# Kernel tuning notes

Hardware: AMD Instinct MI355X
Metric: run time of the kernel (lower is better)

The kernel has to match this reference:

```python
import jax, jax.numpy as jnp
import numpy as np

B, S, H, D, M = 4, 512, 768, 24, 96
OUT_HID = 2 * max(128, H // 2)  # 768

def setup_inputs() -> dict:
    key = jax.random.key(0)
    ks = jax.random.split(key, 10)
    g = lambda k, shp, s=0.02: (jax.random.normal(k, shp, jnp.float32) * s)
    return {
        'H_j': jax.random.normal(ks[0], (B, S, H), jnp.float32),
        'H_i': jax.random.normal(ks[1], (B, S, H), jnp.float32),
        'attn_mask': jnp.ones((B, S), jnp.float32),
        'p_j_w': g(ks[2], (D, H)),
        'p_i_w': g(ks[3], (D, H)),
        's_w1': g(ks[4], (M, 4 * D)),
        's_b1': jnp.zeros((M,), jnp.float32),
        's_w2': g(ks[5], (1, M)),
        's_b2': jnp.zeros((1,), jnp.float32),
        'v_w1': g(ks[6], (OUT_HID, 3 * H)),
        'v_b1': jnp.zeros((OUT_HID,), jnp.float32),
        'v_w2': g(ks[7], (H, OUT_HID)),
        'v_b2': jnp.zeros((H,), jnp.float32),
        'alpha': jnp.asarray(0.05, jnp.float32),
    }

def reference(H_j, H_i, attn_mask, p_j_w, p_i_w, s_w1, s_b1, s_w2, s_b2,
              v_w1, v_b1, v_w2, v_b2, alpha):
    # Projections: [B,S,D]
    Zj = H_j @ p_j_w.T
    Zi = H_i @ p_i_w.T
    # score_mlp layer1 on concat([Zj_pair, Zi_pair, hadam, |diff|]) ==
    # sum of the 4 block-matmuls (block-split of W1 over the concat axis).
    Wa, Wb, Wc, Wd = jnp.split(s_w1, 4, axis=1)        # each [M, D]
    Zj_p = Zj[:, :, None, :]                            # [B,S,1,D]
    Zi_p = Zi[:, None, :, :]                            # [B,1,S,D]
    hid = (jnp.einsum('bsd,md->bsm', Zj, Wa)[:, :, None, :]
           + jnp.einsum('btd,md->btm', Zi, Wb)[:, None, :, :]
           + jnp.einsum('bstd,md->bstm', Zj_p * Zi_p, Wc)
           + jnp.einsum('bstd,md->bstm', jnp.abs(Zj_p - Zi_p), Wd)
           + s_b1)                                      # [B,S,S,M]
    logits = jnp.einsum('bstm,om->bst', jax.nn.relu(hid), s_w2)[..., :] + s_b2[0]  # [B,S,S]
    neg = jnp.finfo(logits.dtype).min
    logits = logits + (1.0 - attn_mask)[:, None, :] * neg  # mask over keys
    probs = jax.nn.softmax(logits, axis=-1)
    ctx = jnp.einsum('bst,bth->bsh', probs, H_i)           # [B,S,H]
    msg_in = jnp.concatenate([ctx, H_j, ctx * H_j], axis=-1)  # concat_hadam: [B,S,3H]
    msg = jax.nn.relu(msg_in @ v_w1.T + v_b1) @ v_w2.T + v_b2
    return alpha * msg  # dropout is identity in eval mode
```

## Files before the change

### kernel.cpp

```cpp
#include <hip/hip_runtime.h>
#include <hip/hip_bf16.h>
#include <math.h>

#define BB 4
#define SS 512
#define HH 768
#define DD 24
#define MM 96
#define OH 768
#define K3H 2304

typedef unsigned short u16;
typedef unsigned int u32;
typedef short bf16x8 __attribute__((ext_vector_type(8)));
typedef float f32x4 __attribute__((ext_vector_type(4)));
typedef u16 u16x4 __attribute__((ext_vector_type(4)));

#define MB_MSGIN  0
#define MB_H1     (MB_MSGIN + BB*SS*K3H)
#define MB_W1     (MB_H1    + BB*SS*OH)
#define MB_W2     (MB_W1    + OH*K3H)
#define MB_PROBS  (MB_W2    + OH*HH)
#define MB_HIT    (MB_PROBS + BB*SS*SS)
#define MB_ZJP    (MB_HIT   + BB*HH*SS)
#define MB_ZIP    (MB_ZJP   + BB*SS*32)
#define MB_WM     (MB_ZIP   + BB*SS*32)
#define MB_WAB    (MB_WM    + MM*96)
#define MB_AB     (MB_WAB   + MM*32)

__device__ inline u16 f2bf(float x) {
    union { float f; u32 u; } v; v.f = x;
    u32 r = v.u + 0x7fffu + ((v.u >> 16) & 1u);
    return (u16)(r >> 16);
}
__device__ inline u32 pk2bf(float lo, float hi) {
    return ((__float_as_uint(lo) + 0x8000u) >> 16) |
           ((__float_as_uint(hi) + 0x8000u) & 0xffff0000u);
}
__device__ inline void unpack8(bf16x8 v, float* f) {
    const u32* d = (const u32*)&v;
    #pragma unroll
    for (int i = 0; i < 4; ++i) {
        f[2*i]   = __uint_as_float(d[i] << 16);
        f[2*i+1] = __uint_as_float(d[i] & 0xffff0000u);
    }
}
__device__ inline void gl_lds16(const u16* g, u16* l) {
    __builtin_amdgcn_global_load_lds(
        (const __attribute__((address_space(1))) void*)g,
        (__attribute__((address_space(3))) void*)l, 16, 0, 0);
}
__device__ inline bf16x8 frag64(const u16* X, int r, int g) {
    return *(const bf16x8*)&X[(r*8 + (g ^ (r & 7)))*8];
}

__global__ __launch_bounds__(256) void k_wm(
    const float* __restrict__ sw1, u16* __restrict__ Wm, u16* __restrict__ Wab)
{
    for (int i = threadIdx.x; i < MM*96; i += 256) {
        int m = i / 96, k = i % 96;
        float v = 0.f;
        if (k < 24)                 v = sw1[m*96 + 48 + k];
        else if (k >= 32 && k < 56) v = sw1[m*96 + 72 + (k - 32)];
        else if (k >= 64 && k < 88) v = sw1[m*96 + 24 + (k - 64)];
        Wm[i] = f2bf(v);
    }
    for (int i = threadIdx.x; i < MM*32; i += 256) {
        int m = i >> 5, k = i & 31;
        Wab[i] = (k < 24) ? f2bf(sw1[m*96 + k]) : (u16)0;
    }
}

#define PZ_END   64
#define PC1_END  928
#define PC2_END  1216
#define PHJ_END  1984
#define PHT_END  2368

__global__ __launch_bounds__(256) void k_prep(
    const float* __restrict__ Hj, const float* __restrict__ Hi,
    const float* __restrict__ pjw, const float* __restrict__ piw,
    const float* __restrict__ sb1,
    const float* __restrict__ vw1, const float* __restrict__ vw2,
    const u16* __restrict__ Wab,
    u16* __restrict__ w1b, u16* __restrict__ w2b,
    u16* __restrict__ Zjp, u16* __restrict__ Zip, u16* __restrict__ Ab,
    u16* __restrict__ msginb, u16* __restrict__ HiTb)
{
    __shared__ __align__(16) u16 smem[5120];
    int bx = blockIdx.x;
    int tid = threadIdx.x;

    if (bx < PZ_END) {
        int idx = bx;
        int isJ = (idx < 32);
        int n0 = (idx & 31) * 64;
        const float* H = isJ ? Hj : Hi;
        const float* P = isJ ? pjw : piw;
        u16* Zout = isJ ? Zjp : Zip;
        u16* As = smem;
        u16* Bs = smem + 2048;
        u16* zb = smem + 3072;
        int wave = tid >> 6, lane = tid & 63;
        int q = lane >> 4, l16 = lane & 15;

        { int i = tid; Bs[(24 + (i >> 5))*32 + (i & 31)] = 0; }

        int arow = tid >> 2, aseg = tid & 3;
        const float* ah = H + (size_t)(n0 + arow)*HH + aseg*8;
        const float* bh = P + (size_t)arow*HH + aseg*8;
        int adst = arow*32 + ((aseg ^ (arow & 3))*8);

        float4 xa = *(const float4*)(ah);
        float4 ya = *(const float4*)(ah + 4);
        float4 xb = {}, yb = {};
        if (tid < 96) { xb = *(const float4*)(bh); yb = *(const float4*)(bh + 4); }

        f32x4 acc0 = {}, acc1 = {};
        int ga = q ^ (l16 & 3);
        for (int k0 = 0; k0 < HH; k0 += 32) {
            { u32* w = (u32*)&As[adst];
              w[0] = pk2bf(xa.x, xa.y); w[1] = pk2bf(xa.z, xa.w);
              w[2] = pk2bf(ya.x, ya.y); w[3] = pk2bf(ya.z, ya.w); }
            if (tid < 96) {
              u32* w = (u32*)&Bs[adst];
              w[0] = pk2bf(xb.x, xb.y); w[1] = pk2bf(xb.z, xb.w);
              w[2] = pk2bf(yb.x, yb.y); w[3] = pk2bf(yb.z, yb.w); }
            float4 nxa = {}, nya = {}, nxb = {}, nyb = {};
            if (k0 + 32 < HH) {
                nxa = *(const float4*)(ah + k0 + 32);
                nya = *(const float4*)(ah + k0 + 36);
                if (tid < 96) { nxb = *(const float4*)(bh + k0 + 32);
                                nyb = *(const float4*)(bh + k0 + 36); }
            }
            __syncthreads();
            bf16x8 af = *(const bf16x8*)&As[(wave*16 + l16)*32 + ga*8];
            bf16x8 b0 = *(const bf16x8*)&Bs[l16*32 + ga*8];
            bf16x8 b1 = *(const bf16x8*)&Bs[(16 + l16)*32 + ga*8];
            acc0 = __builtin_amdgcn_mfma_f32_16x16x32_bf16(af, b0, acc0, 0,0,0);
            acc1 = __builtin_amdgcn_mfma_f32_16x16x32_bf16(af, b1, acc1, 0,0,0);
            __syncthreads();
            xa = nxa; ya = nya; xb = nxb; yb = nyb;
        }
        #pragma unroll
        for (int r = 0; r < 4; ++r) {
            zb[(wave*16 + q*4 + r)*32 + l16]      = f2bf(acc0[r]);
            zb[(wave*16 + q*4 + r)*32 + 16 + l16] = f2bf(acc1[r]);
        }
        __syncthreads();
        { uint4 v = *(const uint4*)&zb[tid*8];
          *(uint4*)&Zout[(size_t)n0*32 + tid*8] = v; }
        if (isJ) {
            bf16x8 af = *(const bf16x8*)&zb[(wave*16 + l16)*32 + q*8];
            #pragma unroll
            for (int nt = 0; nt < 6; ++nt) {
                bf16x8 bw = *(const bf16x8*)&Wab[(nt*16 + l16)*32 + q*8];
                f32x4 a = {};
                a = __builtin_amdgcn_mfma_f32_16x16x32_bf16(af, bw, a, 0,0,0);
                float bv = sb1[nt*16 + l16];
                #pragma unroll
                for (int r = 0; r < 4; ++r) {
                    int bs = n0 + wave*16 + q*4 + r;
                    Ab[(size_t)bs*MM + nt*16 + l16] = f2bf(a[r] + bv);
                }
            }
        }
    } else if (bx < PC2_END) {
        int idx; const float* src; u16* dst;
        if (bx < PC1_END) { idx = bx - PZ_END;  src = vw1; dst = w1b; }
        else              { idx = bx - PC1_END; src = vw2; dst = w2b; }
        int i = (idx*256 + tid) * 8;
        float4 a = *(const float4*)&src[i];
        float4 c = *(const float4*)&src[i+4];
        u16x4 lo = { f2bf(a.x), f2bf(a.y), f2bf(a.z), f2bf(a.w) };
        u16x4 hi = { f2bf(c.x), f2bf(c.y), f2bf(c.z), f2bf(c.w) };
        *(u16x4*)&dst[i]   = lo;
        *(u16x4*)&dst[i+4] = hi;
    } else if (bx < PHJ_END) {
        int idx = bx - PC2_END;
        int e = (idx*256 + tid) * 8;
        int n = e / HH, k = e - n*HH;
        float4 a = *(const float4*)&Hj[e];
        float4 c = *(const float4*)&Hj[e+4];
        u16* dst = msginb + (size_t)n*K3H + HH + k;
        u16x4 lo = { f2bf(a.x), f2bf(a.y), f2bf(a.z), f2bf(a.w) };
        u16x4 hi = { f2bf(c.x), f2bf(c.y), f2bf(c.z), f2bf(c.w) };
        *(u16x4*)&dst[0] = lo;
        *(u16x4*)&dst[4] = hi;
    } else {
        int idx = bx - PHJ_END;
        int t0 = (idx & 7) * 64;
        int h0 = ((idx >> 3) % 12) * 64;
        int b  = idx / 96;
        u16* tile = smem;
        int r = tid >> 2, cs = tid & 3;
        const float* src = Hi + ((size_t)(b*SS) + t0 + r)*HH + h0 + cs*16;
        u16* dst = &tile[r*74 + cs*16];
        #pragma unroll
        for (int i = 0; i < 4; ++i) {
            float4 v = *(const float4*)(src + i*4);
            *(u32*)&dst[i*4]     = pk2bf(v.x, v.y);
            *(u32*)&dst[i*4 + 2] = pk2bf(v.z, v.w);
        }
        __syncthreads();
        int hr = tid >> 2;
        u16 outv[16];
        #pragma unroll
        for (int i = 0; i < 16; ++i) outv[i] = tile[(cs*16 + i)*74 + hr];
        u16* o = HiTb + ((size_t)b*HH + h0 + hr)*SS + t0 + cs*16;
        *(uint4*)o       = *(const uint4*)&outv[0];
        *(uint4*)(o + 8) = *(const uint4*)&outv[8];
    }
}

__global__ __launch_bounds__(256) void k_pair_mfma(
    const u16* __restrict__ Zjp, const u16* __restrict__ Zip,
    const u16* __restrict__ Ab, const u16* __restrict__ Wm,
    const float* __restrict__ sw2, const float* __restrict__ mask,
    u16* __restrict__ probsb)
{
    int blk = blockIdx.x; int b = blk >> 8; int s0 = (blk & 255) * 2;
    int tid = threadIdx.x, wave = tid >> 6, lane = tid & 63;
    int q = lane >> 4, l16 = lane & 15;
    int si = wave & 1, half = wave >> 1;
    int s = s0 + si, bs = b*SS + s;
    __shared__ __align__(16) u16 ZiS[SS*32];
    __shared__ float logits[2][SS];

    {
        const u16* zb = Zip + (size_t)b*SS*32;
        #pragma unroll
        for (int p = 0; p < 8; ++p) {
            int idx = p*256 + tid;
            int t = idx >> 2, c = idx & 3;
            int g = c ^ ((t + (t >> 2)) & 3);
            gl_lds16(zb + t*32 + g*8, ZiS + idx*8);
        }
    }

    bf16x8 zjf = *(const bf16x8*)&Zjp[(size_t)bs*32 + q*8];
    float zj[8]; unpack8(zjf, zj);
    bf16x8 afc[6], afd[6];
    #pragma unroll
    for (int mt = 0; mt < 6; ++mt) {
        const u16* wrow = &Wm[(mt*16 + l16)*96];
        bf16x8 wcf = *(const bf16x8*)&wrow[q*8];
        afd[mt]    = *(const bf16x8*)&wrow[32 + q*8];
        bf16x8 wbf = *(const bf16x8*)&wrow[64 + q*8];
        float fc[8], fb[8];
        unpack8(wcf, fc); unpack8(wbf, fb);
        u32 aval = (u32)Ab[(size_t)bs*MM + mt*16 + l16];
        union { u32 d[4]; bf16x8 v; } pk;
        #pragma unroll
        for (int i = 0; i < 4; ++i)
            pk.d[i] = pk2bf(fmaf(fc[2*i], zj[2*i], fb[2*i]),
                            fmaf(fc[2*i+1], zj[2*i+1], fb[2*i+1]));
        pk.d[0] = (q == 3) ? aval : pk.d[0];
        afc[mt] = pk.v;
    }
    float w2v[6][4];
    #pragma unroll
    for (int mt = 0; mt < 6; ++mt)
        #pragma unroll
        for (int r = 0; r < 4; ++r) w2v[mt][r] = sw2[mt*16 + q*4 + r];

    __syncthreads();

    for (int k = 0; k < 16; ++k) {
        int t0 = (half*16 + k) * 16;
        int trow = t0 + l16;
        int sw = q ^ ((trow + (trow >> 2)) & 3);
        bf16x8 zif = *(const bf16x8*)&ZiS[trow*32 + sw*8];
        float zi[8]; unpack8(zif, zi);
        union { u32 d[4]; bf16x8 v; } b1, b2;
        #pragma unroll
        for (int i = 0; i < 4; ++i)
            b1.d[i] = pk2bf(fabsf(zj[2*i] - zi[2*i]), fabsf(zj[2*i+1] - zi[2*i+1]));
        b2.v = zif;
        b2.d[0] = (q == 3) ? 0x3F80u : b2.d[0];
        f32x4 acc[6];
        #pragma unroll
        for (int mt = 0; mt < 6; ++mt) {
            f32x4 a = {};
            a = __builtin_amdgcn_mfma_f32_16x16x32_bf16(afc[mt], b2.v, a, 0,0,0);
            a = __builtin_amdgcn_mfma_f32_16x16x32_bf16(afd[mt], b1.v, a, 0,0,0);
            acc[mt] = a;
        }
        float p = 0.f;
        #pragma unroll
        for (int mt = 0; mt < 6; ++mt)
            #pragma unroll
            for (int r = 0; r < 4; ++r)
                p = fmaf(fmaxf(acc[mt][r], 0.f), w2v[mt][r], p);
        p += __shfl_xor(p, 16);
        p += __shfl_xor(p, 32);
        if (lane < 16) logits[si][t0 + lane] = p;
    }
    __syncthreads();

    if (wave < 2) {
        const float NEGF = -3.4028234663852886e38f;
        int bss = b*SS + s0 + wave;
        float l[8], e[8];
        float mx = -INFINITY;
        #pragma unroll
        for (int i = 0; i < 8; ++i) {
            int idx = lane + i*64;
            l[i] = logits[wave][idx] + (1.f - mask[b*SS + idx]) * NEGF;
            mx = fmaxf(mx, l[i]);
        }
        #pragma unroll
        for (int off = 32; off > 0; off >>= 1) mx = fmaxf(mx, __shfl_xor(mx, off));
        float sum = 0.f;
        #pragma unroll
        for (int i = 0; i < 8; ++i) { e[i] = __expf(l[i] - mx); sum += e[i]; }
        #pragma unroll
        for (int off = 32; off > 0; off >>= 1) sum += __shfl_xor(sum, off);
        float inv = 1.f / sum;
        #pragma unroll
        for (int i = 0; i < 8; ++i)
            probsb[(size_t)bss*SS + lane + i*64] = f2bf(e[i] * inv);
    }
}

__global__ __launch_bounds__(256) void k_ctx_mfma(
    const u16* __restrict__ probsb, const u16* __restrict__ HiTb,
    u16* __restrict__ msginb)
{
    int b = blockIdx.z;
    int h0 = blockIdx.x * 64;
    int s0 = blockIdx.y * 64;
    int tid = threadIdx.x;
    __shared__ __align__(16) u16 smem[8192];
    u16* As = smem;
    u16* Bs = smem + 4096;
    int wave = tid >> 6, lane = tid & 63;
    int wr = (wave >> 1) * 32, wc = (wave & 1) * 32;
    int q = lane >> 4, l16 = lane & 15;
    f32x4 acc[2][2] = {};
    const u16* ag = probsb + ((size_t)(b*SS) + s0)*SS;
    const u16* bg = HiTb + ((size_t)b*HH + h0)*SS;
    for (int k0 = 0; k0 < SS; k0 += 64) {
        #pragma unroll
        for (int p = 0; p < 2; ++p) {
            int sl = p*256 + tid; int rr = sl >> 3, gi = sl & 7, g = gi ^ (rr & 7);
            gl_lds16(ag + (size_t)rr*SS + k0 + g*8, As + sl*8);
            gl_lds16(bg + (size_t)rr*SS + k0 + g*8, Bs + sl*8);
        }
        __syncthreads();
        #pragma unroll
        for (int ks = 0; ks < 2; ++ks) {
            int g = ks*4 + q;
            bf16x8 a0 = frag64(As, wr + l16, g);
            bf16x8 a1 = frag64(As, wr + 16 + l16, g);
            bf16x8 b0 = frag64(Bs, wc + l16, g);
            bf16x8 b1 = frag64(Bs, wc + 16 + l16, g);
            acc[0][0] = __builtin_amdgcn_mfma_f32_16x16x32_bf16(a0, b0, acc[0][0], 0,0,0);
            acc[0][1] = __builtin_amdgcn_mfma_f32_16x16x32_bf16(a0, b1, acc[0][1], 0,0,0);
            acc[1][0] = __builtin_amdgcn_mfma_f32_16x16x32_bf16(a1, b0, acc[1][0], 0,0,0);
            acc[1][1] = __builtin_amdgcn_mfma_f32_16x16x32_bf16(a1, b1, acc[1][1], 0,0,0);
        }
        __syncthreads();
    }
    u16* zb = smem;
    #pragma unroll
    for (int rt = 0; rt < 2; ++rt)
        #pragma unroll
        for (int ct = 0; ct < 2; ++ct) {
            int hl = wc + ct*16 + l16;
            #pragma unroll
            for (int r = 0; r < 4; ++r)
                zb[(wr + rt*16 + q*4 + r)*72 + hl] = f2bf(acc[rt][ct][r]);
        }
    __syncthreads();
    {
        int s_l = tid >> 2, seg = tid & 3;
        u16 cv[16], hv[16], pv[16];
        *(uint4*)&cv[0] = *(const uint4*)&zb[s_l*72 + seg*16];
        *(uint4*)&cv[8] = *(const uint4*)&zb[s_l*72 + seg*16 + 8];
        u16* row = msginb + (size_t)(b*SS + s0 + s_l)*K3H;
        int hc = h0 + seg*16;
        *(uint4*)&hv[0] = *(const uint4*)&row[HH + hc];
        *(uint4*)&hv[8] = *(const uint4*)&row[HH + hc + 8];
        #pragma unroll
        for (int i = 0; i < 8; ++i) {
            float c0 = __uint_as_float((u32)cv[2*i] << 16);
            float c1 = __uint_as_float((u32)cv[2*i+1] << 16);
            float g0 = __uint_as_float((u32)hv[2*i] << 16);
            float g1 = __uint_as_float((u32)hv[2*i+1] << 16);
            u32 pr = pk2bf(c0*g0, c1*g1);
            pv[2*i] = (u16)pr; pv[2*i+1] = (u16)(pr >> 16);
        }
        *(uint4*)&row[hc]     = *(const uint4*)&cv[0];
        *(uint4*)&row[hc + 8] = *(const uint4*)&cv[8];
        *(uint4*)&row[2*HH + hc]     = *(const uint4*)&pv[0];
        *(uint4*)&row[2*HH + hc + 8] = *(const uint4*)&pv[8];
    }
}

__global__ __launch_bounds__(256) void k_mfma_gemm1(
    const u16* __restrict__ Abf, const u16* __restrict__ Bbf,
    const float* __restrict__ bias, u16* __restrict__ Cbf)
{
    int o0 = blockIdx.x * 64;
    int n0 = blockIdx.y * 64;
    int tid = threadIdx.x;
    __shared__ __align__(16) u16 As[64*64];
    __shared__ __align__(16) u16 Bs[64*64];
    int wave = tid >> 6, lane = tid & 63;
    int wr = (wave >> 1) * 32, wc = (wave & 1) * 32;
    int q = lane >> 4, l16 = lane & 15;
    f32x4 acc[2][2] = {};
    const u16* ag = Abf + (size_t)n0*K3H;
    const u16* bg = Bbf + (size_t)o0*K3H;
    for (int k0 = 0; k0 < K3H; k0 += 64) {
        #pragma unroll
        for (int p = 0; p < 2; ++p) {
            int sl = p*256 + tid; int rr = sl >> 3, gi = sl & 7, g = gi ^ (rr & 7);
            gl_lds16(ag + (size_t)rr*K3H + k0 + g*8, As + sl*8);
            gl_lds16(bg + (size_t)rr*K3H + k0 + g*8, Bs + sl*8);
        }
        __syncthreads();
        #pragma unroll
        for (int ks = 0; ks < 2; ++ks) {
            int g = ks*4 + q;
            bf16x8 a0 = frag64(As, wr + l16, g);
            bf16x8 a1 = frag64(As, wr + 16 + l16, g);
            bf16x8 b0 = frag64(Bs, wc + l16, g);
            bf16x8 b1 = frag64(Bs, wc + 16 + l16, g);
            acc[0][0] = __builtin_amdgcn_mfma_f32_16x16x32_bf16(a0, b0, acc[0][0], 0,0,0);
            acc[0][1] = __builtin_amdgcn_mfma_f32_16x16x32_bf16(a0, b1, acc[0][1], 0,0,0);
            acc[1][0] = __builtin_amdgcn_mfma_f32_16x16x32_bf16(a1, b0, acc[1][0], 0,0,0);
            acc[1][1] = __builtin_amdgcn_mfma_f32_16x16x32_bf16(a1, b1, acc[1][1], 0,0,0);
        }
        __syncthreads();
    }
    #pragma unroll
    for (int rt = 0; rt < 2; ++rt) {
        #pragma unroll
        for (int ct = 0; ct < 2; ++ct) {
            int o = o0 + wc + ct*16 + l16;
            float bv = bias[o];
            #pragma unroll
            for (int r = 0; r < 4; ++r) {
                int m = n0 + wr + rt*16 + q*4 + r;
                Cbf[(size_t)m*OH + o] = f2bf(fmaxf(acc[rt][ct][r] + bv, 0.f));
            }
        }
    }
}

__global__ __launch_bounds__(256) void k_mfma_gemm2(
    const u16* __restrict__ Abf, const u16* __restrict__ Bbf,
    const float* __restrict__ bias, const float* __restrict__ alpha,
    float* __restrict__ out)
{
    int o0 = blockIdx.x * 64;
    int n0 = blockIdx.y * 64;
    int tid = threadIdx.x;
    __shared__ __align__(16) u16 As[64*64];
    __shared__ __align__(16) u16 Bs[64*64];
    int wave = tid >> 6, lane = tid & 63;
    int wr = (wave >> 1) * 32, wc = (wave & 1) * 32;
    int q = lane >> 4, l16 = lane & 15;
    f32x4 acc[2][2] = {};
    const u16* ag = Abf + (size_t)n0*OH;
    const u16* bg = Bbf + (size_t)o0*OH;
    for (int k0 = 0; k0 < OH; k0 += 64) {
        #pragma unroll
        for (int p = 0; p < 2; ++p) {
            int sl = p*256 + tid; int rr = sl >> 3, gi = sl & 7, g = gi ^ (rr & 7);
            gl_lds16(ag + (size_t)rr*OH + k0 + g*8, As + sl*8);
            gl_lds16(bg + (size_t)rr*OH + k0 + g*8, Bs + sl*8);
        }
        __syncthreads();
        #pragma unroll
        for (int ks = 0; ks < 2; ++ks) {
            int g = ks*4 + q;
            bf16x8 a0 = frag64(As, wr + l16, g);
            bf16x8 a1 = frag64(As, wr + 16 + l16, g);
            bf16x8 b0 = frag64(Bs, wc + l16, g);
            bf16x8 b1 = frag64(Bs, wc + 16 + l16, g);
            acc[0][0] = __builtin_amdgcn_mfma_f32_16x16x32_bf16(a0, b0, acc[0][0], 0,0,0);
            acc[0][1] = __builtin_amdgcn_mfma_f32_16x16x32_bf16(a0, b1, acc[0][1], 0,0,0);
            acc[1][0] = __builtin_amdgcn_mfma_f32_16x16x32_bf16(a1, b0, acc[1][0], 0,0,0);
            acc[1][1] = __builtin_amdgcn_mfma_f32_16x16x32_bf16(a1, b1, acc[1][1], 0,0,0);
        }
        __syncthreads();
    }
    float al = alpha[0];
    #pragma unroll
    for (int rt = 0; rt < 2; ++rt) {
        #pragma unroll
        for (int ct = 0; ct < 2; ++ct) {
            int o = o0 + wc + ct*16 + l16;
            float bv = bias[o];
            #pragma unroll
            for (int r = 0; r < 4; ++r) {
                int m = n0 + wr + rt*16 + q*4 + r;
                out[(size_t)m*HH + o] = al * (acc[rt][ct][r] + bv);
            }
        }
    }
}

extern "C" void kernel_launch(void* const* d_in, const int* in_sizes, int n_in,
                              void* d_out, int out_size, void* d_ws, size_t ws_size,
                              hipStream_t stream) {
    const float* Hj    = (const float*)d_in[0];
    const float* Hi    = (const float*)d_in[1];
    const float* amask = (const float*)d_in[2];
    const float* pjw   = (const float*)d_in[3];
    const float* piw   = (const float*)d_in[4];
    const float* sw1   = (const float*)d_in[5];
    const float* sb1   = (const float*)d_in[6];
    const float* sw2   = (const float*)d_in[7];
    const float* sb2   = (const float*)d_in[8];
    const float* vw1   = (const float*)d_in[9];
    const float* vb1   = (const float*)d_in[10];
    const float* vw2   = (const float*)d_in[11];
    const float* vb2   = (const float*)d_in[12];
    const float* alpha = (const float*)d_in[13];
    float* out = (float*)d_out;
    (void)sb2;

    u16* bfbase = (u16*)d_ws;
    u16* msginb = bfbase + MB_MSGIN;
    u16* h1b    = bfbase + MB_H1;
    u16* w1b    = bfbase + MB_W1;
    u16* w2b    = bfbase + MB_W2;
    u16* probsb = bfbase + MB_PROBS;
    u16* hitb   = bfbase + MB_HIT;
    u16* zjp    = bfbase + MB_ZJP;
    u16* zip    = bfbase + MB_ZIP;
    u16* wm     = bfbase + MB_WM;
    u16* wab    = bfbase + MB_WAB;
    u16* ab     = bfbase + MB_AB;

    k_wm<<<1, 256, 0, stream>>>(sw1, wm, wab);
    k_prep<<<PHT_END, 256, 0, stream>>>(Hj, Hi, pjw, piw, sb1, vw1, vw2, wab,
                                        w1b, w2b, zjp, zip, ab, msginb, hitb);
    k_pair_mfma<<<BB*SS/2, 256, 0, stream>>>(zjp, zip, ab, wm, sw2, amask, probsb);
    k_ctx_mfma<<<dim3(HH/64, SS/64, BB), 256, 0, stream>>>(probsb, hitb, msginb);
    k_mfma_gemm1<<<dim3(OH/64, BB*SS/64), 256, 0, stream>>>(msginb, w1b, vb1, h1b);
    k_mfma_gemm2<<<dim3(HH/64, BB*SS/64), 256, 0, stream>>>(h1b, w2b, vb2, alpha, out);
}
```

Before: 191.0 us.

## Load GEMM B fragments directly from global and fuse Hj bf16 conversion into ctx

The three MFMA GEMM kernels no longer stage the B operand in LDS. Each wave now reads its bf16x8 B fragments straight from global memory, relying on L2/cache reuse across blocks and cutting LDS traffic and footprint. Separately, the Hj-to-bf16 copy into msg_in is removed from the prep kernel and done in the ctx epilogue, which reads fp32 Hj directly and writes all three msg_in segments. This drops a launch slice and a round trip through msg_in, but the B loads become uncoalesced, strided per-lane global reads inside the inner loop.

Result: slower. 229.1 us (+19.9%).

```diff
diff --git a/kernel.cpp b/kernel.cpp
--- a/kernel.cpp
+++ b/kernel.cpp
@@ -74,8 +74,7 @@
 #define PZ_END   64
 #define PC1_END  928
 #define PC2_END  1216
-#define PHJ_END  1984
-#define PHT_END  2368
+#define PHT_END  1600
 
 __global__ __launch_bounds__(256) void k_prep(
     const float* __restrict__ Hj, const float* __restrict__ Hi,
@@ -85,7 +84,7 @@
     const u16* __restrict__ Wab,
     u16* __restrict__ w1b, u16* __restrict__ w2b,
     u16* __restrict__ Zjp, u16* __restrict__ Zip, u16* __restrict__ Ab,
-    u16* __restrict__ msginb, u16* __restrict__ HiTb)
+    u16* __restrict__ HiTb)
 {
     __shared__ __align__(16) u16 smem[5120];
     int bx = blockIdx.x;
@@ -176,19 +175,8 @@
         u16x4 hi = { f2bf(c.x), f2bf(c.y), f2bf(c.z), f2bf(c.w) };
         *(u16x4*)&dst[i]   = lo;
         *(u16x4*)&dst[i+4] = hi;
-    } else if (bx < PHJ_END) {
+    } else {
         int idx = bx - PC2_END;
-        int e = (idx*256 + tid) * 8;
-        int n = e / HH, k = e - n*HH;
-        float4 a = *(const float4*)&Hj[e];
-        float4 c = *(const float4*)&Hj[e+4];
-        u16* dst = msginb + (size_t)n*K3H + HH + k;
-        u16x4 lo = { f2bf(a.x), f2bf(a.y), f2bf(a.z), f2bf(a.w) };
-        u16x4 hi = { f2bf(c.x), f2bf(c.y), f2bf(c.z), f2bf(c.w) };
-        *(u16x4*)&dst[0] = lo;
-        *(u16x4*)&dst[4] = hi;
-    } else {
-        int idx = bx - PHJ_END;
         int t0 = (idx & 7) * 64;
         int h0 = ((idx >> 3) % 12) * 64;
         int b  = idx / 96;
@@ -325,27 +313,26 @@
 
 __global__ __launch_bounds__(256) void k_ctx_mfma(
     const u16* __restrict__ probsb, const u16* __restrict__ HiTb,
-    u16* __restrict__ msginb)
+    const float* __restrict__ Hj, u16* __restrict__ msginb)
 {
     int b = blockIdx.z;
     int h0 = blockIdx.x * 64;
     int s0 = blockIdx.y * 64;
     int tid = threadIdx.x;
-    __shared__ __align__(16) u16 smem[8192];
+    __shared__ __align__(16) u16 smem[4608];
     u16* As = smem;
-    u16* Bs = smem + 4096;
     int wave = tid >> 6, lane = tid & 63;
     int wr = (wave >> 1) * 32, wc = (wave & 1) * 32;
     int q = lane >> 4, l16 = lane & 15;
     f32x4 acc[2][2] = {};
     const u16* ag = probsb + ((size_t)(b*SS) + s0)*SS;
-    const u16* bg = HiTb + ((size_t)b*HH + h0)*SS;
+    const u16* bg0 = HiTb + ((size_t)b*HH + h0 + wc + l16)*SS + q*8;
+    const u16* bg1 = bg0 + (size_t)16*SS;
     for (int k0 = 0; k0 < SS; k0 += 64) {
         #pragma unroll
         for (int p = 0; p < 2; ++p) {
             int sl = p*256 + tid; int rr = sl >> 3, gi = sl & 7, g = gi ^ (rr & 7);
             gl_lds16(ag + (size_t)rr*SS + k0 + g*8, As + sl*8);
-            gl_lds16(bg + (size_t)rr*SS + k0 + g*8, Bs + sl*8);
         }
         __syncthreads();
         #pragma unroll
@@ -353,8 +340,8 @@
             int g = ks*4 + q;
             bf16x8 a0 = frag64(As, wr + l16, g);
             bf16x8 a1 = frag64(As, wr + 16 + l16, g);
-            bf16x8 b0 = frag64(Bs, wc + l16, g);
-            bf16x8 b1 = frag64(Bs, wc + 16 + l16, g);
+            bf16x8 b0 = *(const bf16x8*)(bg0 + k0 + ks*32);
+            bf16x8 b1 = *(const bf16x8*)(bg1 + k0 + ks*32);
             acc[0][0] = __builtin_amdgcn_mfma_f32_16x16x32_bf16(a0, b0, acc[0][0], 0,0,0);
             acc[0][1] = __builtin_amdgcn_mfma_f32_16x16x32_bf16(a0, b1, acc[0][1], 0,0,0);
             acc[1][0] = __builtin_amdgcn_mfma_f32_16x16x32_bf16(a1, b0, acc[1][0], 0,0,0);
@@ -378,21 +365,27 @@
         u16 cv[16], hv[16], pv[16];
         *(uint4*)&cv[0] = *(const uint4*)&zb[s_l*72 + seg*16];
         *(uint4*)&cv[8] = *(const uint4*)&zb[s_l*72 + seg*16 + 8];
-        u16* row = msginb + (size_t)(b*SS + s0 + s_l)*K3H;
         int hc = h0 + seg*16;
-        *(uint4*)&hv[0] = *(const uint4*)&row[HH + hc];
-        *(uint4*)&hv[8] = *(const uint4*)&row[HH + hc + 8];
+        const float* hj = Hj + ((size_t)(b*SS) + s0 + s_l)*HH + hc;
+        float hf[16];
+        #pragma unroll
+        for (int i = 0; i < 4; ++i) *(float4*)&hf[i*4] = *(const float4*)(hj + i*4);
         #pragma unroll
         for (int i = 0; i < 8; ++i) {
             float c0 = __uint_as_float((u32)cv[2*i] << 16);
             float c1 = __uint_as_float((u32)cv[2*i+1] << 16);
+            u32 hr = pk2bf(hf[2*i], hf[2*i+1]);
+            hv[2*i] = (u16)hr; hv[2*i+1] = (u16)(hr >> 16);
             float g0 = __uint_as_float((u32)hv[2*i] << 16);
             float g1 = __uint_as_float((u32)hv[2*i+1] << 16);
             u32 pr = pk2bf(c0*g0, c1*g1);
             pv[2*i] = (u16)pr; pv[2*i+1] = (u16)(pr >> 16);
         }
-        *(uint4*)&row[hc]     = *(const uint4*)&cv[0];
-        *(uint4*)&row[hc + 8] = *(const uint4*)&cv[8];
+        u16* row = msginb + (size_t)(b*SS + s0 + s_l)*K3H;
+        *(uint4*)&row[hc]            = *(const uint4*)&cv[0];
+        *(uint4*)&row[hc + 8]        = *(const uint4*)&cv[8];
+        *(uint4*)&row[HH + hc]       = *(const uint4*)&hv[0];
+        *(uint4*)&row[HH + hc + 8]   = *(const uint4*)&hv[8];
         *(uint4*)&row[2*HH + hc]     = *(const uint4*)&pv[0];
         *(uint4*)&row[2*HH + hc + 8] = *(const uint4*)&pv[8];
     }
@@ -406,19 +399,18 @@
     int n0 = blockIdx.y * 64;
     int tid = threadIdx.x;
     __shared__ __align__(16) u16 As[64*64];
-    __shared__ __align__(16) u16 Bs[64*64];
     int wave = tid >> 6, lane = tid & 63;
     int wr = (wave >> 1) * 32, wc = (wave & 1) * 32;
     int q = lane >> 4, l16 = lane & 15;
     f32x4 acc[2][2] = {};
     const u16* ag = Abf + (size_t)n0*K3H;
-    const u16* bg = Bbf + (size_t)o0*K3H;
+    const u16* bg0 = Bbf + (size_t)(o0 + wc + l16)*K3H + q*8;
+    const u16* bg1 = bg0 + (size_t)16*K3H;
     for (int k0 = 0; k0 < K3H; k0 += 64) {
         #pragma unroll
         for (int p = 0; p < 2; ++p) {
             int sl = p*256 + tid; int rr = sl >> 3, gi = sl & 7, g = gi ^ (rr & 7);
             gl_lds16(ag + (size_t)rr*K3H + k0 + g*8, As + sl*8);
-            gl_lds16(bg + (size_t)rr*K3H + k0 + g*8, Bs + sl*8);
         }
         __syncthreads();
         #pragma unroll
@@ -426,8 +418,8 @@
             int g = ks*4 + q;
             bf16x8 a0 = frag64(As, wr + l16, g);
             bf16x8 a1 = frag64(As, wr + 16 + l16, g);
-            bf16x8 b0 = frag64(Bs, wc + l16, g);
-            bf16x8 b1 = frag64(Bs, wc + 16 + l16, g);
+            bf16x8 b0 = *(const bf16x8*)(bg0 + k0 + ks*32);
+            bf16x8 b1 = *(const bf16x8*)(bg1 + k0 + ks*32);
             acc[0][0] = __builtin_amdgcn_mfma_f32_16x16x32_bf16(a0, b0, acc[0][0], 0,0,0);
             acc[0][1] = __builtin_amdgcn_mfma_f32_16x16x32_bf16(a0, b1, acc[0][1], 0,0,0);
             acc[1][0] = __builtin_amdgcn_mfma_f32_16x16x32_bf16(a1, b0, acc[1][0], 0,0,0);
@@ -459,19 +451,18 @@
     int n0 = blockIdx.y * 64;
     int tid = threadIdx.x;
     __shared__ __align__(16) u16 As[64*64];
-    __shared__ __align__(16) u16 Bs[64*64];
     int wave = tid >> 6, lane = tid & 63;
     int wr = (wave >> 1) * 32, wc = (wave & 1) * 32;
     int q = lane >> 4, l16 = lane & 15;
     f32x4 acc[2][2] = {};
     const u16* ag = Abf + (size_t)n0*OH;
-    const u16* bg = Bbf + (size_t)o0*OH;
+    const u16* bg0 = Bbf + (size_t)(o0 + wc + l16)*OH + q*8;
+    const u16* bg1 = bg0 + (size_t)16*OH;
     for (int k0 = 0; k0 < OH; k0 += 64) {
         #pragma unroll
         for (int p = 0; p < 2; ++p) {
             int sl = p*256 + tid; int rr = sl >> 3, gi = sl & 7, g = gi ^ (rr & 7);
             gl_lds16(ag + (size_t)rr*OH + k0 + g*8, As + sl*8);
-            gl_lds16(bg + (size_t)rr*OH + k0 + g*8, Bs + sl*8);
         }
         __syncthreads();
         #pragma unroll
@@ -479,8 +470,8 @@
             int g = ks*4 + q;
             bf16x8 a0 = frag64(As, wr + l16, g);
             bf16x8 a1 = frag64(As, wr + 16 + l16, g);
-            bf16x8 b0 = frag64(Bs, wc + l16, g);
-            bf16x8 b1 = frag64(Bs, wc + 16 + l16, g);
+            bf16x8 b0 = *(const bf16x8*)(bg0 + k0 + ks*32);
+            bf16x8 b1 = *(const bf16x8*)(bg1 + k0 + ks*32);
             acc[0][0] = __builtin_amdgcn_mfma_f32_16x16x32_bf16(a0, b0, acc[0][0], 0,0,0);
             acc[0][1] = __builtin_amdgcn_mfma_f32_16x16x32_bf16(a0, b1, acc[0][1], 0,0,0);
             acc[1][0] = __builtin_amdgcn_mfma_f32_16x16x32_bf16(a1, b0, acc[1][0], 0,0,0);
@@ -539,9 +530,9 @@
 
     k_wm<<<1, 256, 0, stream>>>(sw1, wm, wab);
     k_prep<<<PHT_END, 256, 0, stream>>>(Hj, Hi, pjw, piw, sb1, vw1, vw2, wab,
-                                        w1b, w2b, zjp, zip, ab, msginb, hitb);
+                                        w1b, w2b, zjp, zip, ab, hitb);
     k_pair_mfma<<<BB*SS/2, 256, 0, stream>>>(zjp, zip, ab, wm, sw2, amask, probsb);
-    k_ctx_mfma<<<dim3(HH/64, SS/64, BB), 256, 0, stream>>>(probsb, hitb, msginb);
+    k_ctx_mfma<<<dim3(HH/64, SS/64, BB), 256, 0, stream>>>(probsb, hitb, Hj, msginb);
     k_mfma_gemm1<<<dim3(OH/64, BB*SS/64), 256, 0, stream>>>(msginb, w1b, vb1, h1b);
     k_mfma_gemm2<<<dim3(HH/64, BB*SS/64), 256, 0, stream>>>(h1b, w2b, vb2, alpha, out);
 }
```
